# Optimization experiments

Hardware: AMD Instinct MI355X
Metric: run time of the kernel (lower is better)

Reference implementation:

```python
import jax, jax.numpy as jnp
import numpy as np
from jax import lax

SEQ_LENGTH = 32
B, I, O = 1024, 2048, 1024
DT = 1e-3
TAU_PRE, TAU_POST = 0.02, 0.02
ETA_PLUS, ETA_MINUS = 1e-3, 1e-3
W_MIN, W_MAX = -1.0, 1.0
TAU_MEM = 0.02
V_TH = 1.0


def setup_inputs() -> dict:
    key = jax.random.key(0)
    k1, k2, k3 = jax.random.split(key, 3)
    # Bernoulli(0.05) input spikes, rate-coded, reused each timestep
    input_spikes = (jax.random.uniform(k1, (B, I)) < 0.05).astype(jnp.float32)
    weight = jax.random.normal(k2, (O, I), dtype=jnp.float32) * (1.0 / np.sqrt(I))
    bias = jax.random.normal(k3, (O,), dtype=jnp.float32) * 0.01
    return {"input_spikes": input_spikes, "weight": weight, "bias": bias}


def reference(input_spikes, weight, bias):
    decay_pre = jnp.exp(jnp.float32(-DT / TAU_PRE))
    decay_post = jnp.exp(jnp.float32(-DT / TAU_POST))
    v_decay = jnp.exp(jnp.float32(-DT / TAU_MEM))

    b = input_spikes.shape[0]
    v0 = jnp.zeros((b, O), dtype=input_spikes.dtype)
    z0 = jnp.zeros((b, O), dtype=input_spikes.dtype)
    # STDPState(t_pre=1.0, t_post=1.0) broadcast to trace shapes
    tpre0 = jnp.ones((b, I), dtype=input_spikes.dtype)
    tpost0 = jnp.ones((b, O), dtype=input_spikes.dtype)

    def step(carry, _):
        v, w, tpre, tpost, _z = carry
        # linear projection with current (plastic) weights
        z_in = input_spikes @ w.T + bias  # [B, O]
        # LIF output neuron: decay, integrate, threshold, reset
        v = v * v_decay + z_in
        z_out = (v >= V_TH).astype(v.dtype)
        v = v * (1.0 - z_out)
        # STDP trace update: decay then accumulate spikes
        tpre = tpre * decay_pre + input_spikes
        tpost = tpost * decay_post + z_out
        # spike-gated eligibility outer products, summed over batch
        dw = (ETA_PLUS * jnp.einsum('bo,bi->oi', z_out, tpre)
              - ETA_MINUS * jnp.einsum('bo,bi->oi', tpost, input_spikes))
        w = jnp.clip(w + dw, W_MIN, W_MAX)
        return (v, w, tpre, tpost, z_out), None

    (v, w, tpre, tpost, z_out), _ = lax.scan(
        step, (v0, weight, tpre0, tpost0, z0), None, length=SEQ_LENGTH)
    return z_out, v, w
```

## Files before the change

### kernel.cpp

```cpp
#include <hip/hip_runtime.h>
#include <cmath>

#define SEQ 32
#define BB 1024
#define II 2048
#define OO 1024

typedef unsigned short ushortt;

__global__ void build_idx_rev(const float* __restrict__ x, ushortt* __restrict__ idxArr,
                              int* __restrict__ cntArr, int* __restrict__ rcnt,
                              ushortt* __restrict__ rev) {
  int b = blockIdx.x;
  int lane = threadIdx.x;
  __shared__ ushortt sIdx[256];
  const float* row = x + (long)b * II;
  int base = 0;
  for (int c = 0; c < II / 64; ++c) {
    float val = row[c * 64 + lane];
    unsigned long long m = __ballot(val != 0.0f);
    if (val != 0.0f) {
      int pos = base + __popcll(m & ((1ull << lane) - 1ull));
      if (pos < 256) {
        idxArr[(b << 8) + pos] = (ushortt)(c * 64 + lane);
        sIdx[pos] = (ushortt)(c * 64 + lane);
      }
    }
    base += __popcll(m);
  }
  int cnt = base < 256 ? base : 256;
  if (lane == 0) cntArr[b] = cnt;
  __syncthreads();
  for (int j = lane; j < cnt; j += 64) {
    int i = sIdx[j];
    int pos = atomicAdd(&rcnt[i], 1);
    if (pos < 128) rev[((long)i << 7) + pos] = (ushortt)b;
  }
}

__global__ void build_idxT(const ushortt* __restrict__ idxArr, const int* __restrict__ cntArr,
                           ushortt* __restrict__ idxT, const int* __restrict__ rcnt,
                           float* __restrict__ nvec) {
  int id = blockIdx.x * 256 + threadIdx.x;
  int j = id >> 10, b = id & 1023;
  idxT[id] = (j < cntArr[b]) ? idxArr[(b << 8) + j] : (ushortt)II;
  if (id < II) nvec[id] = (float)rcnt[id];
}

__global__ void transpose_f32(const float* __restrict__ src, float* __restrict__ dst,
                              int R, int C) {
  __shared__ float t[32][33];
  int c0 = blockIdx.x * 32, r0 = blockIdx.y * 32;
  int tx = threadIdx.x, ty = threadIdx.y;
#pragma unroll
  for (int k = 0; k < 4; k++)
    t[ty + k * 8][tx] = src[(long)(r0 + ty + k * 8) * C + c0 + tx];
  __syncthreads();
#pragma unroll
  for (int k = 0; k < 4; k++)
    dst[(long)(c0 + ty + k * 8) * R + r0 + tx] = t[tx][ty + k * 8];
}

__global__ void transpose2_f32(const float* __restrict__ zC, const float* __restrict__ vC,
                               float* __restrict__ oz, float* __restrict__ ov) {
  __shared__ float t[32][33];
  const float* src = blockIdx.z ? vC : zC;
  float* dst = blockIdx.z ? ov : oz;
  int c0 = blockIdx.x * 32, r0 = blockIdx.y * 32;
  int tx = threadIdx.x, ty = threadIdx.y;
#pragma unroll
  for (int k = 0; k < 4; k++)
    t[ty + k * 8][tx] = src[(long)(r0 + ty + k * 8) * BB + c0 + tx];
  __syncthreads();
#pragma unroll
  for (int k = 0; k < 4; k++)
    dst[(long)(c0 + ty + k * 8) * OO + r0 + tx] = t[tx][ty + k * 8];
}

__global__ __launch_bounds__(256) void s0_kernel(
    const float* __restrict__ wT, const ushortt* __restrict__ idxArr,
    const int* __restrict__ cntArr, const float* __restrict__ nvec,
    float* __restrict__ S0, float* __restrict__ snArr) {
  int b = blockIdx.x, tid = threadIdx.x, lane = tid & 63, wave = tid >> 6;
  __shared__ ushortt sIdx[256];
  __shared__ float sred[4];
  sIdx[tid] = idxArr[(b << 8) + tid];
  __syncthreads();
  int cnt = cntArr[b];
  const float4* wT4 = (const float4*)wT;
  float4 acc; acc.x = acc.y = acc.z = acc.w = 0.f;
  int j = 0;
  for (; j + 4 <= cnt; j += 4) {
    int i0 = sIdx[j], i1 = sIdx[j + 1], i2 = sIdx[j + 2], i3 = sIdx[j + 3];
    float4 a0 = wT4[(i0 << 8) + tid];
    float4 a1 = wT4[(i1 << 8) + tid];
    float4 a2 = wT4[(i2 << 8) + tid];
    float4 a3 = wT4[(i3 << 8) + tid];
    acc.x += a0.x; acc.y += a0.y; acc.z += a0.z; acc.w += a0.w;
    acc.x += a1.x; acc.y += a1.y; acc.z += a1.z; acc.w += a1.w;
    acc.x += a2.x; acc.y += a2.y; acc.z += a2.z; acc.w += a2.w;
    acc.x += a3.x; acc.y += a3.y; acc.z += a3.z; acc.w += a3.w;
  }
  for (; j < cnt; ++j) {
    float4 a = wT4[((int)sIdx[j] << 8) + tid];
    acc.x += a.x; acc.y += a.y; acc.z += a.z; acc.w += a.w;
  }
  ((float4*)S0)[(b << 8) + tid] = acc;
  float sv = (tid < cnt) ? nvec[sIdx[tid]] : 0.f;
#pragma unroll
  for (int off = 32; off > 0; off >>= 1) sv += __shfl_xor(sv, off);
  if (lane == 0) sred[wave] = sv;
  __syncthreads();
  if (tid == 0) snArr[b] = sred[0] + sred[1] + sred[2] + sred[3];
}

__global__ __launch_bounds__(512, 8) void snn_kernel(
    const float* __restrict__ w,
    const float* __restrict__ bias, const float* __restrict__ nvec,
    const ushortt* __restrict__ idxT, const int* __restrict__ cntArr,
    const float* __restrict__ snArr, const float* __restrict__ S0T,
    const int* __restrict__ rcnt, const ushortt* __restrict__ rev,
    const ushortt* __restrict__ idxArr,
    float* __restrict__ zC, float* __restrict__ vC, float* __restrict__ outw,
    float dec) {
  int o = blockIdx.x, tid = threadIdx.x, lane = tid & 63, wave = tid >> 6;
  __shared__ float shbuf[9219];
  __shared__ int sCnt, sFlag, cFlag;
  float* wL = shbuf;
  float* aG = shbuf + 2049;
  float* nG = shbuf + 4098;
  float* mL = shbuf + 6147;
  int* sList = (int*)(shbuf + 8195);
  float* Sfix = shbuf + 6147;
  float* SnuD = shbuf + 7171;
  float* SAD = shbuf + 8195;

#pragma unroll
  for (int q = 0; q < 4; ++q) {
    int i = q * 512 + tid;
    wL[i] = w[(long)o * II + i];
    aG[i] = 0.f;
    nG[i] = nvec[i];
  }
  if (tid == 0) {
    sFlag = 0; cFlag = 0;
    wL[II] = 0.f; aG[II] = 0.f; nG[II] = 0.f;
  }

  double S[2];
  float Snu[2], SA[2], v4[2], zo4[2], vo4[2];
#pragma unroll
  for (int k = 0; k < 2; ++k) {
    int b = k * 512 + tid;
    S[k] = (double)S0T[(long)o * BB + b];
    Snu[k] = snArr[b];
    SA[k] = 0.f;
    v4[k] = 0.f; zo4[k] = 0.f; vo4[k] = 0.f;
    Sfix[b] = 0.f; SnuD[b] = 0.f; SAD[b] = 0.f;
  }
  int jmax[2];
#pragma unroll
  for (int k = 0; k < 2; ++k) {
    int c = cntArr[k * 512 + wave * 64 + lane];
#pragma unroll
    for (int off = 32; off > 0; off >>= 1) c = max(c, __shfl_xor(c, off));
    jmax[k] = c;
  }
  float bo = bias[o];
  unsigned clipped = 0;
  bool everSpk = false;
  float p = 1.f, u = 1.f;
  __syncthreads();

  for (int t = 0; t < SEQ; ++t) {
    p *= dec; u *= dec; u += 1.f;
    float spre = u - p;
    int local = 0;
    float zk[2];
#pragma unroll
    for (int k = 0; k < 2; ++k) {
      float zin = (float)S[k] + bo;
      float nv = v4[k] * dec + zin;
      float z = (nv >= 1.f) ? 1.f : 0.f;
      nv = nv * (1.f - z);
      v4[k] = nv; zk[k] = z;
      if (z != 0.f) local = 1;
    }
    if (local) sFlag = 1;
    __syncthreads();
    int spk = sFlag;

    if (!spk) {
#pragma unroll
      for (int q = 0; q < 4; ++q) {
        int i = q * 512 + tid;
        bool already = (clipped >> q) & 1u;
        float n = 0.f, atn = 0.f, fix = 0.f;
        bool cl = false;
        if (!already) {
          n = nG[i];
          atn = everSpk ? (dec * aG[i]) : 0.f;
          float dw = -(1e-3f * (p * n + atn));
          float wold = wL[i];
          float pre = wold + dw;
          float wv = fminf(fmaxf(pre, -1.f), 1.f);
          cl = (pre <= -1.f);
          if (cl) {
            clipped |= 1u << q;
            fix = (-1.f - wold) - dw;
            nG[i] = 0.f;
            if (everSpk) aG[i] = 0.f;
          } else if (everSpk) {
            aG[i] = atn;
          }
          wL[i] = wv;
        }
        unsigned long long m = __ballot(cl);
        if (m) {
          if (lane == 0) cFlag = 1;
          while (m) {
            int src = __builtin_ctzll(m);
            m &= m - 1;
            int ii = __shfl(i, src);
            float fx = __shfl(fix, src);
            float mn = -__shfl(n, src);
            float ma = -__shfl(atn, src);
            int rc = rcnt[ii];
            const ushortt* rp = rev + ((long)ii << 7);
            for (int r = lane; r < rc; r += 64) {
              int b = rp[r];
              atomicAdd(&Sfix[b], fx);
              atomicAdd(&SnuD[b], mn);
              if (everSpk) atomicAdd(&SAD[b], ma);
            }
          }
        }
      }
      __syncthreads();
      float coefP = 1e-3f * p;
      if (cFlag) {
#pragma unroll
        for (int k = 0; k < 2; ++k) {
          int b = k * 512 + tid;
          S[k] = S[k] - (double)coefP * (double)Snu[k]
                      - (double)1e-3f * (double)(dec * SA[k])
                      + (double)Sfix[b];
          SA[k] = dec * SA[k] + SAD[b];
          Snu[k] = Snu[k] + SnuD[b];
          Sfix[b] = 0.f; SnuD[b] = 0.f; SAD[b] = 0.f;
        }
      } else {
#pragma unroll
        for (int k = 0; k < 2; ++k) {
          S[k] = S[k] - (double)coefP * (double)Snu[k]
                      - (double)1e-3f * (double)(dec * SA[k]);
          SA[k] = dec * SA[k];
        }
      }
      if (tid == 0) { sFlag = 0; cFlag = 0; }
      __syncthreads();
    } else {
      everSpk = true;
      if (tid == 0) sCnt = 0;
      __syncthreads();
#pragma unroll
      for (int k = 0; k < 2; ++k)
        if (zk[k] != 0.f) { int pos = atomicAdd(&sCnt, 1); sList[pos] = k * 512 + tid; }
#pragma unroll
      for (int q = 0; q < 4; ++q) mL[q * 512 + tid] = 0.f;
      __syncthreads();
      int ns = sCnt;
      for (int s = wave; s < ns; s += 8) {
        int b = sList[s];
        int cb = cntArr[b];
        const ushortt* ip = idxArr + (b << 8);
        for (int j = lane; j < cb; j += 64)
          atomicAdd(&mL[ip[j]], 1.f);
      }
      __syncthreads();
      float cv = (float)ns;
#pragma unroll
      for (int q = 0; q < 4; ++q) {
        int i = q * 512 + tid;
        float mt = mL[i];
        float atn = dec * aG[i] + mt;
        float n = nvec[i];
        float dw = 1e-3f * (p * cv + spre * mt) - 1e-3f * (p * n + atn);
        float wold = wL[i];
        float pre = wold + dw;
        float wv = fminf(fmaxf(pre, -1.f), 1.f);
        bool cl = (pre <= -1.f);
        if (cl) clipped |= 1u << q; else clipped &= ~(1u << q);
        wL[i] = wv;
        aG[i] = cl ? 0.f : atn;
        nG[i] = cl ? 0.f : n;
      }
      __syncthreads();
#pragma unroll
      for (int k = 0; k < 2; ++k) {
        int b = k * 512 + tid;
        double s = 0.0;
        float sa = 0.f, sn = 0.f;
        int jm = jmax[k];
        int j = 0;
        for (; j + 4 <= jm; j += 4) {
          int i0 = idxT[(long)j * BB + b];
          int i1 = idxT[(long)(j + 1) * BB + b];
          int i2 = idxT[(long)(j + 2) * BB + b];
          int i3 = idxT[(long)(j + 3) * BB + b];
          s += (double)wL[i0]; sa += aG[i0]; sn += nG[i0];
          s += (double)wL[i1]; sa += aG[i1]; sn += nG[i1];
          s += (double)wL[i2]; sa += aG[i2]; sn += nG[i2];
          s += (double)wL[i3]; sa += aG[i3]; sn += nG[i3];
        }
        for (; j < jm; ++j) {
          int idx = idxT[(long)j * BB + b];
          s += (double)wL[idx]; sa += aG[idx]; sn += nG[idx];
        }
        S[k] = s; SA[k] = sa; Snu[k] = sn;
      }
#pragma unroll
      for (int k = 0; k < 2; ++k) {
        int b = k * 512 + tid;
        Sfix[b] = 0.f; SnuD[b] = 0.f; SAD[b] = 0.f;
      }
      if (tid == 0) { sFlag = 0; cFlag = 0; }
      __syncthreads();
    }

    if (t == SEQ - 1) {
#pragma unroll
      for (int k = 0; k < 2; ++k) { zo4[k] = zk[k]; vo4[k] = v4[k]; }
    }
  }

  __syncthreads();
#pragma unroll
  for (int q = 0; q < 4; ++q) outw[(long)o * II + q * 512 + tid] = wL[q * 512 + tid];
#pragma unroll
  for (int k = 0; k < 2; ++k) {
    int b = k * 512 + tid;
    zC[(long)o * BB + b] = zo4[k];
    vC[(long)o * BB + b] = vo4[k];
  }
}

extern "C" void kernel_launch(void* const* d_in, const int* in_sizes, int n_in,
                              void* d_out, int out_size, void* d_ws, size_t ws_size,
                              hipStream_t stream) {
  const float* x = (const float*)d_in[0];
  const float* w = (const float*)d_in[1];
  const float* bias = (const float*)d_in[2];
  float* out = (float*)d_out;

  char* ws = (char*)d_ws;
  ushortt* idxArr = (ushortt*)(ws + 0);
  int* cntArr = (int*)(ws + 524288);
  ushortt* idxT = (ushortt*)(ws + 528384);
  float* nvec = (float*)(ws + 1052672);
  float* snArr = (float*)(ws + 1060864);
  int* rcnt = (int*)(ws + 1064960);
  ushortt* rev = (ushortt*)(ws + 1073152);
  float* wT = (float*)(ws + 1597440);
  float* S0 = (float*)(ws + 9986048);
  float* S0T = (float*)(ws + 14180352);
  float* zC = (float*)(ws + 18374656);
  float* vC = (float*)(ws + 22568960);

  hipMemsetAsync(rcnt, 0, II * sizeof(int), stream);
  build_idx_rev<<<BB, 64, 0, stream>>>(x, idxArr, cntArr, rcnt, rev);
  build_idxT<<<1024, 256, 0, stream>>>(idxArr, cntArr, idxT, rcnt, nvec);
  transpose_f32<<<dim3(II / 32, OO / 32), dim3(32, 8), 0, stream>>>(w, wT, OO, II);
  s0_kernel<<<BB, 256, 0, stream>>>(wT, idxArr, cntArr, nvec, S0, snArr);
  transpose_f32<<<dim3(OO / 32, BB / 32), dim3(32, 8), 0, stream>>>(S0, S0T, BB, OO);

  const float dec = (float)exp(-0.05);

  snn_kernel<<<OO, 512, 0, stream>>>(w, bias, nvec, idxT, cntArr, snArr, S0T,
                                     rcnt, rev, idxArr, zC, vC, out + 2 * BB * OO, dec);

  transpose2_f32<<<dim3(BB / 32, OO / 32, 2), dim3(32, 8), 0, stream>>>(zC, vC, out, out + BB * OO);
}
```

Before: 290.6 us.

## Interleave weight/trace arrays into float4 LDS records and pack index transpose by fours

Packs the per-input weight, eligibility trace, pre-count and scratch accumulator into a single float4 shared-memory record. The sparse gather can then fetch all three values with one 128-bit LDS read instead of three scattered reads. The transposed index array is re-laid out so each thread loads four indices at once as a ushort4. The change also removes the everSpk branch, reuses the float4 w-slot as scratch for the per-batch fix accumulators, and merges the sCnt reset into the existing barrier. Shared memory footprint grows, to about 36KB, which may reduce occupancy. Aliasing the scratch slots across different roles is also a correctness risk.

```diff
diff --git a/kernel.cpp b/kernel.cpp
--- a/kernel.cpp
+++ b/kernel.cpp
@@ -43,7 +43,8 @@
                            float* __restrict__ nvec) {
   int id = blockIdx.x * 256 + threadIdx.x;
   int j = id >> 10, b = id & 1023;
-  idxT[id] = (j < cntArr[b]) ? idxArr[(b << 8) + j] : (ushortt)II;
+  ushortt v = (j < cntArr[b]) ? idxArr[(b << 8) + j] : (ushortt)II;
+  idxT[(j >> 2) * 4096 + (b << 2) + (j & 3)] = v;
   if (id < II) nvec[id] = (float)rcnt[id];
 }
 
@@ -124,39 +125,33 @@
     float* __restrict__ zC, float* __restrict__ vC, float* __restrict__ outw,
     float dec) {
   int o = blockIdx.x, tid = threadIdx.x, lane = tid & 63, wave = tid >> 6;
-  __shared__ float shbuf[9219];
+  __shared__ float4 wan[II + 1];
+  __shared__ float SAD[BB];
+  __shared__ ushortt sList[BB];
   __shared__ int sCnt, sFlag, cFlag;
-  float* wL = shbuf;
-  float* aG = shbuf + 2049;
-  float* nG = shbuf + 4098;
-  float* mL = shbuf + 6147;
-  int* sList = (int*)(shbuf + 8195);
-  float* Sfix = shbuf + 6147;
-  float* SnuD = shbuf + 7171;
-  float* SAD = shbuf + 8195;
+  float* wf = (float*)wan;
 
 #pragma unroll
   for (int q = 0; q < 4; ++q) {
     int i = q * 512 + tid;
-    wL[i] = w[(long)o * II + i];
-    aG[i] = 0.f;
-    nG[i] = nvec[i];
-  }
+    wan[i] = make_float4(w[(long)o * II + i], 0.f, nvec[i], 0.f);
+  }
+#pragma unroll
+  for (int k = 0; k < 2; ++k) SAD[k * 512 + tid] = 0.f;
   if (tid == 0) {
-    sFlag = 0; cFlag = 0;
-    wL[II] = 0.f; aG[II] = 0.f; nG[II] = 0.f;
+    sFlag = 0; cFlag = 0; sCnt = 0;
+    wan[II] = make_float4(0.f, 0.f, 0.f, 0.f);
   }
 
   double S[2];
-  float Snu[2], SA[2], v4[2], zo4[2], vo4[2];
+  float Snu[2], SA[2], v4[2], zk[2];
 #pragma unroll
   for (int k = 0; k < 2; ++k) {
     int b = k * 512 + tid;
     S[k] = (double)S0T[(long)o * BB + b];
     Snu[k] = snArr[b];
     SA[k] = 0.f;
-    v4[k] = 0.f; zo4[k] = 0.f; vo4[k] = 0.f;
-    Sfix[b] = 0.f; SnuD[b] = 0.f; SAD[b] = 0.f;
+    v4[k] = 0.f; zk[k] = 0.f;
   }
   int jmax[2];
 #pragma unroll
@@ -168,7 +163,6 @@
   }
   float bo = bias[o];
   unsigned clipped = 0;
-  bool everSpk = false;
   float p = 1.f, u = 1.f;
   __syncthreads();
 
@@ -176,7 +170,6 @@
     p *= dec; u *= dec; u += 1.f;
     float spre = u - p;
     int local = 0;
-    float zk[2];
 #pragma unroll
     for (int k = 0; k < 2; ++k) {
       float zin = (float)S[k] + bo;
@@ -187,6 +180,7 @@
       if (z != 0.f) local = 1;
     }
     if (local) sFlag = 1;
+    if (tid == 0) sCnt = 0;
     __syncthreads();
     int spk = sFlag;
 
@@ -198,22 +192,24 @@
         float n = 0.f, atn = 0.f, fix = 0.f;
         bool cl = false;
         if (!already) {
-          n = nG[i];
-          atn = everSpk ? (dec * aG[i]) : 0.f;
+          float4 tq = wan[i];
+          n = tq.z;
+          atn = dec * tq.y;
           float dw = -(1e-3f * (p * n + atn));
-          float wold = wL[i];
+          float wold = tq.x;
           float pre = wold + dw;
           float wv = fminf(fmaxf(pre, -1.f), 1.f);
           cl = (pre <= -1.f);
+          float ny, nz;
           if (cl) {
             clipped |= 1u << q;
             fix = (-1.f - wold) - dw;
-            nG[i] = 0.f;
-            if (everSpk) aG[i] = 0.f;
-          } else if (everSpk) {
-            aG[i] = atn;
+            ny = 0.f; nz = 0.f;
+          } else {
+            ny = atn; nz = n;
           }
-          wL[i] = wv;
+          *(float2*)&wan[i] = make_float2(wv, ny);
+          ((float*)&wan[i])[2] = nz;
         }
         unsigned long long m = __ballot(cl);
         if (m) {
@@ -228,10 +224,10 @@
             int rc = rcnt[ii];
             const ushortt* rp = rev + ((long)ii << 7);
             for (int r = lane; r < rc; r += 64) {
-              int b = rp[r];
-              atomicAdd(&Sfix[b], fx);
-              atomicAdd(&SnuD[b], mn);
-              if (everSpk) atomicAdd(&SAD[b], ma);
+              int b2 = rp[r];
+              atomicAdd(&wf[(b2 << 2) + 3], fx);
+              atomicAdd(&wf[((1024 + b2) << 2) + 3], mn);
+              atomicAdd(&SAD[b2], ma);
             }
           }
         }
@@ -242,12 +238,15 @@
 #pragma unroll
         for (int k = 0; k < 2; ++k) {
           int b = k * 512 + tid;
+          float fx = wf[(b << 2) + 3];
+          float snd = wf[((1024 + b) << 2) + 3];
+          float sad = SAD[b];
           S[k] = S[k] - (double)coefP * (double)Snu[k]
                       - (double)1e-3f * (double)(dec * SA[k])
-                      + (double)Sfix[b];
-          SA[k] = dec * SA[k] + SAD[b];
-          Snu[k] = Snu[k] + SnuD[b];
-          Sfix[b] = 0.f; SnuD[b] = 0.f; SAD[b] = 0.f;
+                      + (double)fx;
+          SA[k] = dec * SA[k] + sad;
+          Snu[k] = Snu[k] + snd;
+          wf[(b << 2) + 3] = 0.f; wf[((1024 + b) << 2) + 3] = 0.f; SAD[b] = 0.f;
         }
       } else {
 #pragma unroll
@@ -260,14 +259,9 @@
       if (tid == 0) { sFlag = 0; cFlag = 0; }
       __syncthreads();
     } else {
-      everSpk = true;
-      if (tid == 0) sCnt = 0;
-      __syncthreads();
 #pragma unroll
       for (int k = 0; k < 2; ++k)
-        if (zk[k] != 0.f) { int pos = atomicAdd(&sCnt, 1); sList[pos] = k * 512 + tid; }
-#pragma unroll
-      for (int q = 0; q < 4; ++q) mL[q * 512 + tid] = 0.f;
+        if (zk[k] != 0.f) { int pos = atomicAdd(&sCnt, 1); sList[pos] = (ushortt)(k * 512 + tid); }
       __syncthreads();
       int ns = sCnt;
       for (int s = wave; s < ns; s += 8) {
@@ -275,73 +269,69 @@
         int cb = cntArr[b];
         const ushortt* ip = idxArr + (b << 8);
         for (int j = lane; j < cb; j += 64)
-          atomicAdd(&mL[ip[j]], 1.f);
+          atomicAdd(&wf[((int)ip[j] << 2) + 3], 1.f);
       }
       __syncthreads();
       float cv = (float)ns;
 #pragma unroll
       for (int q = 0; q < 4; ++q) {
         int i = q * 512 + tid;
-        float mt = mL[i];
-        float atn = dec * aG[i] + mt;
-        float n = nvec[i];
-        float dw = 1e-3f * (p * cv + spre * mt) - 1e-3f * (p * n + atn);
-        float wold = wL[i];
-        float pre = wold + dw;
+        float4 tq = wan[i];
+        float mt = tq.w;
+        float atn = dec * tq.y + mt;
+        float n0 = nvec[i];
+        float dw = 1e-3f * (p * cv + spre * mt) - 1e-3f * (p * n0 + atn);
+        float pre = tq.x + dw;
         float wv = fminf(fmaxf(pre, -1.f), 1.f);
         bool cl = (pre <= -1.f);
         if (cl) clipped |= 1u << q; else clipped &= ~(1u << q);
-        wL[i] = wv;
-        aG[i] = cl ? 0.f : atn;
-        nG[i] = cl ? 0.f : n;
-      }
-      __syncthreads();
+        wan[i] = make_float4(wv, cl ? 0.f : atn, cl ? 0.f : n0, 0.f);
+      }
+      __syncthreads();
+      const ushort4* tpb = (const ushort4*)idxT;
 #pragma unroll
       for (int k = 0; k < 2; ++k) {
         int b = k * 512 + tid;
         double s = 0.0;
         float sa = 0.f, sn = 0.f;
-        int jm = jmax[k];
-        int j = 0;
-        for (; j + 4 <= jm; j += 4) {
-          int i0 = idxT[(long)j * BB + b];
-          int i1 = idxT[(long)(j + 1) * BB + b];
-          int i2 = idxT[(long)(j + 2) * BB + b];
-          int i3 = idxT[(long)(j + 3) * BB + b];
-          s += (double)wL[i0]; sa += aG[i0]; sn += nG[i0];
-          s += (double)wL[i1]; sa += aG[i1]; sn += nG[i1];
-          s += (double)wL[i2]; sa += aG[i2]; sn += nG[i2];
-          s += (double)wL[i3]; sa += aG[i3]; sn += nG[i3];
-        }
-        for (; j < jm; ++j) {
-          int idx = idxT[(long)j * BB + b];
-          s += (double)wL[idx]; sa += aG[idx]; sn += nG[idx];
+        int jm4 = (jmax[k] + 3) >> 2;
+        const ushort4* tp = tpb + b;
+        int g = 0;
+        for (; g + 2 <= jm4; g += 2) {
+          ushort4 u0 = tp[(g << 10)];
+          ushort4 u1 = tp[((g + 1) << 10)];
+          float4 a0 = wan[u0.x], a1 = wan[u0.y], a2 = wan[u0.z], a3 = wan[u0.w];
+          s += (double)a0.x; s += (double)a1.x; s += (double)a2.x; s += (double)a3.x;
+          sa += a0.y; sa += a1.y; sa += a2.y; sa += a3.y;
+          sn += a0.z; sn += a1.z; sn += a2.z; sn += a3.z;
+          float4 b0 = wan[u1.x], b1 = wan[u1.y], b2 = wan[u1.z], b3 = wan[u1.w];
+          s += (double)b0.x; s += (double)b1.x; s += (double)b2.x; s += (double)b3.x;
+          sa += b0.y; sa += b1.y; sa += b2.y; sa += b3.y;
+          sn += b0.z; sn += b1.z; sn += b2.z; sn += b3.z;
+        }
+        for (; g < jm4; ++g) {
+          ushort4 u0 = tp[(g << 10)];
+          float4 a0 = wan[u0.x], a1 = wan[u0.y], a2 = wan[u0.z], a3 = wan[u0.w];
+          s += (double)a0.x; s += (double)a1.x; s += (double)a2.x; s += (double)a3.x;
+          sa += a0.y; sa += a1.y; sa += a2.y; sa += a3.y;
+          sn += a0.z; sn += a1.z; sn += a2.z; sn += a3.z;
         }
         S[k] = s; SA[k] = sa; Snu[k] = sn;
-      }
-#pragma unroll
-      for (int k = 0; k < 2; ++k) {
-        int b = k * 512 + tid;
-        Sfix[b] = 0.f; SnuD[b] = 0.f; SAD[b] = 0.f;
+        SAD[b] = 0.f;
       }
       if (tid == 0) { sFlag = 0; cFlag = 0; }
       __syncthreads();
     }
-
-    if (t == SEQ - 1) {
-#pragma unroll
-      for (int k = 0; k < 2; ++k) { zo4[k] = zk[k]; vo4[k] = v4[k]; }
-    }
-  }
-
-  __syncthreads();
-#pragma unroll
-  for (int q = 0; q < 4; ++q) outw[(long)o * II + q * 512 + tid] = wL[q * 512 + tid];
+  }
+
+  __syncthreads();
+#pragma unroll
+  for (int q = 0; q < 4; ++q) outw[(long)o * II + q * 512 + tid] = wan[q * 512 + tid].x;
 #pragma unroll
   for (int k = 0; k < 2; ++k) {
     int b = k * 512 + tid;
-    zC[(long)o * BB + b] = zo4[k];
-    vC[(long)o * BB + b] = vo4[k];
+    zC[(long)o * BB + b] = zk[k];
+    vC[(long)o * BB + b] = v4[k];
   }
 }
 
```

Measured after the change: 314.7 us. 1.08x slower.

## Fold initial projection and index transpose into main kernels, drop prep passes

Applied to the files above, without the earlier changes.

Removes the weight transpose, the separate S0 gather kernel, its output transpose and the build_idxT pass. The initial per-batch sum and spike-count sum are now computed inside the main kernel from the shared-memory weight row. The transposed spike index table is written directly by build_idx_rev in a ushort4-packed layout, and the per-step gather reads four indices per load. This cuts several kernel launches and global-memory round trips, at the cost of an extra gather phase at the start of every output block. The padded index layout now assumes at most 256 spikes per row, split into 64 groups of 4.

```diff
diff --git a/kernel.cpp b/kernel.cpp
--- a/kernel.cpp
+++ b/kernel.cpp
@@ -10,7 +10,7 @@
 
 __global__ void build_idx_rev(const float* __restrict__ x, ushortt* __restrict__ idxArr,
                               int* __restrict__ cntArr, int* __restrict__ rcnt,
-                              ushortt* __restrict__ rev) {
+                              ushortt* __restrict__ rev, ushortt* __restrict__ idxT) {
   int b = blockIdx.x;
   int lane = threadIdx.x;
   __shared__ ushortt sIdx[256];
@@ -31,34 +31,20 @@
   int cnt = base < 256 ? base : 256;
   if (lane == 0) cntArr[b] = cnt;
   __syncthreads();
+  {
+    int j0 = lane * 4;
+    ushort4 u;
+    u.x = (j0 + 0 < cnt) ? sIdx[j0 + 0] : (ushortt)II;
+    u.y = (j0 + 1 < cnt) ? sIdx[j0 + 1] : (ushortt)II;
+    u.z = (j0 + 2 < cnt) ? sIdx[j0 + 2] : (ushortt)II;
+    u.w = (j0 + 3 < cnt) ? sIdx[j0 + 3] : (ushortt)II;
+    ((ushort4*)idxT)[(lane << 10) + b] = u;
+  }
   for (int j = lane; j < cnt; j += 64) {
     int i = sIdx[j];
     int pos = atomicAdd(&rcnt[i], 1);
     if (pos < 128) rev[((long)i << 7) + pos] = (ushortt)b;
   }
-}
-
-__global__ void build_idxT(const ushortt* __restrict__ idxArr, const int* __restrict__ cntArr,
-                           ushortt* __restrict__ idxT, const int* __restrict__ rcnt,
-                           float* __restrict__ nvec) {
-  int id = blockIdx.x * 256 + threadIdx.x;
-  int j = id >> 10, b = id & 1023;
-  idxT[id] = (j < cntArr[b]) ? idxArr[(b << 8) + j] : (ushortt)II;
-  if (id < II) nvec[id] = (float)rcnt[id];
-}
-
-__global__ void transpose_f32(const float* __restrict__ src, float* __restrict__ dst,
-                              int R, int C) {
-  __shared__ float t[32][33];
-  int c0 = blockIdx.x * 32, r0 = blockIdx.y * 32;
-  int tx = threadIdx.x, ty = threadIdx.y;
-#pragma unroll
-  for (int k = 0; k < 4; k++)
-    t[ty + k * 8][tx] = src[(long)(r0 + ty + k * 8) * C + c0 + tx];
-  __syncthreads();
-#pragma unroll
-  for (int k = 0; k < 4; k++)
-    dst[(long)(c0 + ty + k * 8) * R + r0 + tx] = t[tx][ty + k * 8];
 }
 
 __global__ void transpose2_f32(const float* __restrict__ zC, const float* __restrict__ vC,
@@ -77,48 +63,9 @@
     dst[(long)(c0 + ty + k * 8) * OO + r0 + tx] = t[tx][ty + k * 8];
 }
 
-__global__ __launch_bounds__(256) void s0_kernel(
-    const float* __restrict__ wT, const ushortt* __restrict__ idxArr,
-    const int* __restrict__ cntArr, const float* __restrict__ nvec,
-    float* __restrict__ S0, float* __restrict__ snArr) {
-  int b = blockIdx.x, tid = threadIdx.x, lane = tid & 63, wave = tid >> 6;
-  __shared__ ushortt sIdx[256];
-  __shared__ float sred[4];
-  sIdx[tid] = idxArr[(b << 8) + tid];
-  __syncthreads();
-  int cnt = cntArr[b];
-  const float4* wT4 = (const float4*)wT;
-  float4 acc; acc.x = acc.y = acc.z = acc.w = 0.f;
-  int j = 0;
-  for (; j + 4 <= cnt; j += 4) {
-    int i0 = sIdx[j], i1 = sIdx[j + 1], i2 = sIdx[j + 2], i3 = sIdx[j + 3];
-    float4 a0 = wT4[(i0 << 8) + tid];
-    float4 a1 = wT4[(i1 << 8) + tid];
-    float4 a2 = wT4[(i2 << 8) + tid];
-    float4 a3 = wT4[(i3 << 8) + tid];
-    acc.x += a0.x; acc.y += a0.y; acc.z += a0.z; acc.w += a0.w;
-    acc.x += a1.x; acc.y += a1.y; acc.z += a1.z; acc.w += a1.w;
-    acc.x += a2.x; acc.y += a2.y; acc.z += a2.z; acc.w += a2.w;
-    acc.x += a3.x; acc.y += a3.y; acc.z += a3.z; acc.w += a3.w;
-  }
-  for (; j < cnt; ++j) {
-    float4 a = wT4[((int)sIdx[j] << 8) + tid];
-    acc.x += a.x; acc.y += a.y; acc.z += a.z; acc.w += a.w;
-  }
-  ((float4*)S0)[(b << 8) + tid] = acc;
-  float sv = (tid < cnt) ? nvec[sIdx[tid]] : 0.f;
-#pragma unroll
-  for (int off = 32; off > 0; off >>= 1) sv += __shfl_xor(sv, off);
-  if (lane == 0) sred[wave] = sv;
-  __syncthreads();
-  if (tid == 0) snArr[b] = sred[0] + sred[1] + sred[2] + sred[3];
-}
-
 __global__ __launch_bounds__(512, 8) void snn_kernel(
-    const float* __restrict__ w,
-    const float* __restrict__ bias, const float* __restrict__ nvec,
+    const float* __restrict__ w, const float* __restrict__ bias,
     const ushortt* __restrict__ idxT, const int* __restrict__ cntArr,
-    const float* __restrict__ snArr, const float* __restrict__ S0T,
     const int* __restrict__ rcnt, const ushortt* __restrict__ rev,
     const ushortt* __restrict__ idxArr,
     float* __restrict__ zC, float* __restrict__ vC, float* __restrict__ outw,
@@ -140,24 +87,18 @@
     int i = q * 512 + tid;
     wL[i] = w[(long)o * II + i];
     aG[i] = 0.f;
-    nG[i] = nvec[i];
+    nG[i] = (float)rcnt[i];
+  }
+#pragma unroll
+  for (int k = 0; k < 2; ++k) {
+    int b = k * 512 + tid;
+    Sfix[b] = 0.f; SnuD[b] = 0.f; SAD[b] = 0.f;
   }
   if (tid == 0) {
     sFlag = 0; cFlag = 0;
     wL[II] = 0.f; aG[II] = 0.f; nG[II] = 0.f;
   }
 
-  double S[2];
-  float Snu[2], SA[2], v4[2], zo4[2], vo4[2];
-#pragma unroll
-  for (int k = 0; k < 2; ++k) {
-    int b = k * 512 + tid;
-    S[k] = (double)S0T[(long)o * BB + b];
-    Snu[k] = snArr[b];
-    SA[k] = 0.f;
-    v4[k] = 0.f; zo4[k] = 0.f; vo4[k] = 0.f;
-    Sfix[b] = 0.f; SnuD[b] = 0.f; SAD[b] = 0.f;
-  }
   int jmax[2];
 #pragma unroll
   for (int k = 0; k < 2; ++k) {
@@ -172,11 +113,30 @@
   float p = 1.f, u = 1.f;
   __syncthreads();
 
+  const ushort4* tpb = (const ushort4*)idxT;
+  double S[2];
+  float Snu[2], SA[2], v4[2], zk[2];
+#pragma unroll
+  for (int k = 0; k < 2; ++k) {
+    int b = k * 512 + tid;
+    double s = 0.0;
+    float sn = 0.f;
+    int jm4 = (jmax[k] + 3) >> 2;
+    const ushort4* tp = tpb + b;
+    for (int g = 0; g < jm4; ++g) {
+      ushort4 u0 = tp[(g << 10)];
+      int a_ = u0.x, b_ = u0.y, c_ = u0.z, d_ = u0.w;
+      s += (double)wL[a_]; s += (double)wL[b_]; s += (double)wL[c_]; s += (double)wL[d_];
+      sn += nG[a_]; sn += nG[b_]; sn += nG[c_]; sn += nG[d_];
+    }
+    S[k] = s; Snu[k] = sn;
+    SA[k] = 0.f; v4[k] = 0.f; zk[k] = 0.f;
+  }
+
   for (int t = 0; t < SEQ; ++t) {
     p *= dec; u *= dec; u += 1.f;
     float spre = u - p;
     int local = 0;
-    float zk[2];
 #pragma unroll
     for (int k = 0; k < 2; ++k) {
       float zin = (float)S[k] + bo;
@@ -228,10 +188,10 @@
             int rc = rcnt[ii];
             const ushortt* rp = rev + ((long)ii << 7);
             for (int r = lane; r < rc; r += 64) {
-              int b = rp[r];
-              atomicAdd(&Sfix[b], fx);
-              atomicAdd(&SnuD[b], mn);
-              if (everSpk) atomicAdd(&SAD[b], ma);
+              int b2 = rp[r];
+              atomicAdd(&Sfix[b2], fx);
+              atomicAdd(&SnuD[b2], mn);
+              if (everSpk) atomicAdd(&SAD[b2], ma);
             }
           }
         }
@@ -284,7 +244,7 @@
         int i = q * 512 + tid;
         float mt = mL[i];
         float atn = dec * aG[i] + mt;
-        float n = nvec[i];
+        float n = (float)rcnt[i];
         float dw = 1e-3f * (p * cv + spre * mt) - 1e-3f * (p * n + atn);
         float wold = wL[i];
         float pre = wold + dw;
@@ -301,21 +261,30 @@
         int b = k * 512 + tid;
         double s = 0.0;
         float sa = 0.f, sn = 0.f;
-        int jm = jmax[k];
-        int j = 0;
-        for (; j + 4 <= jm; j += 4) {
-          int i0 = idxT[(long)j * BB + b];
-          int i1 = idxT[(long)(j + 1) * BB + b];
-          int i2 = idxT[(long)(j + 2) * BB + b];
-          int i3 = idxT[(long)(j + 3) * BB + b];
-          s += (double)wL[i0]; sa += aG[i0]; sn += nG[i0];
-          s += (double)wL[i1]; sa += aG[i1]; sn += nG[i1];
-          s += (double)wL[i2]; sa += aG[i2]; sn += nG[i2];
-          s += (double)wL[i3]; sa += aG[i3]; sn += nG[i3];
-        }
-        for (; j < jm; ++j) {
-          int idx = idxT[(long)j * BB + b];
-          s += (double)wL[idx]; sa += aG[idx]; sn += nG[idx];
+        int jm4 = (jmax[k] + 3) >> 2;
+        const ushort4* tp = tpb + b;
+        int g = 0;
+        for (; g + 2 <= jm4; g += 2) {
+          ushort4 u0 = tp[(g << 10)];
+          ushort4 u1 = tp[((g + 1) << 10)];
+          int a_ = u0.x, b_ = u0.y, c_ = u0.z, d_ = u0.w;
+          s += (double)wL[a_]; sa += aG[a_]; sn += nG[a_];
+          s += (double)wL[b_]; sa += aG[b_]; sn += nG[b_];
+          s += (double)wL[c_]; sa += aG[c_]; sn += nG[c_];
+          s += (double)wL[d_]; sa += aG[d_]; sn += nG[d_];
+          int e_ = u1.x, f_ = u1.y, g_ = u1.z, h_ = u1.w;
+          s += (double)wL[e_]; sa += aG[e_]; sn += nG[e_];
+          s += (double)wL[f_]; sa += aG[f_]; sn += nG[f_];
+          s += (double)wL[g_]; sa += aG[g_]; sn += nG[g_];
+          s += (double)wL[h_]; sa += aG[h_]; sn += nG[h_];
+        }
+        for (; g < jm4; ++g) {
+          ushort4 u0 = tp[(g << 10)];
+          int a_ = u0.x, b_ = u0.y, c_ = u0.z, d_ = u0.w;
+          s += (double)wL[a_]; sa += aG[a_]; sn += nG[a_];
+          s += (double)wL[b_]; sa += aG[b_]; sn += nG[b_];
+          s += (double)wL[c_]; sa += aG[c_]; sn += nG[c_];
+          s += (double)wL[d_]; sa += aG[d_]; sn += nG[d_];
         }
         S[k] = s; SA[k] = sa; Snu[k] = sn;
       }
@@ -327,11 +296,6 @@
       if (tid == 0) { sFlag = 0; cFlag = 0; }
       __syncthreads();
     }
-
-    if (t == SEQ - 1) {
-#pragma unroll
-      for (int k = 0; k < 2; ++k) { zo4[k] = zk[k]; vo4[k] = v4[k]; }
-    }
   }
 
   __syncthreads();
@@ -340,8 +304,8 @@
 #pragma unroll
   for (int k = 0; k < 2; ++k) {
     int b = k * 512 + tid;
-    zC[(long)o * BB + b] = zo4[k];
-    vC[(long)o * BB + b] = vo4[k];
+    zC[(long)o * BB + b] = zk[k];
+    vC[(long)o * BB + b] = v4[k];
   }
 }
 
@@ -357,27 +321,18 @@
   ushortt* idxArr = (ushortt*)(ws + 0);
   int* cntArr = (int*)(ws + 524288);
   ushortt* idxT = (ushortt*)(ws + 528384);
-  float* nvec = (float*)(ws + 1052672);
-  float* snArr = (float*)(ws + 1060864);
-  int* rcnt = (int*)(ws + 1064960);
-  ushortt* rev = (ushortt*)(ws + 1073152);
-  float* wT = (float*)(ws + 1597440);
-  float* S0 = (float*)(ws + 9986048);
-  float* S0T = (float*)(ws + 14180352);
-  float* zC = (float*)(ws + 18374656);
-  float* vC = (float*)(ws + 22568960);
+  int* rcnt = (int*)(ws + 1052672);
+  ushortt* rev = (ushortt*)(ws + 1060864);
+  float* zC = (float*)(ws + 1585152);
+  float* vC = (float*)(ws + 5779456);
 
   hipMemsetAsync(rcnt, 0, II * sizeof(int), stream);
-  build_idx_rev<<<BB, 64, 0, stream>>>(x, idxArr, cntArr, rcnt, rev);
-  build_idxT<<<1024, 256, 0, stream>>>(idxArr, cntArr, idxT, rcnt, nvec);
-  transpose_f32<<<dim3(II / 32, OO / 32), dim3(32, 8), 0, stream>>>(w, wT, OO, II);
-  s0_kernel<<<BB, 256, 0, stream>>>(wT, idxArr, cntArr, nvec, S0, snArr);
-  transpose_f32<<<dim3(OO / 32, BB / 32), dim3(32, 8), 0, stream>>>(S0, S0T, BB, OO);
+  build_idx_rev<<<BB, 64, 0, stream>>>(x, idxArr, cntArr, rcnt, rev, idxT);
 
   const float dec = (float)exp(-0.05);
 
-  snn_kernel<<<OO, 512, 0, stream>>>(w, bias, nvec, idxT, cntArr, snArr, S0T,
-                                     rcnt, rev, idxArr, zC, vC, out + 2 * BB * OO, dec);
+  snn_kernel<<<OO, 512, 0, stream>>>(w, bias, idxT, cntArr, rcnt, rev, idxArr,
+                                     zC, vC, out + 2 * BB * OO, dec);
 
   transpose2_f32<<<dim3(BB / 32, OO / 32, 2), dim3(32, 8), 0, stream>>>(zC, vC, out, out + BB * OO);
 }
```

After: 285.6 us. Within noise of the previous version (-1.7%).
